# Optimization experiments

Measured on AMD Instinct MI355X. Metric: run time of the kernel, lower is better.

The kernel has to match this reference:

```python
import jax, jax.numpy as jnp
import numpy as np

N = 1_000_000          # points
C_IN = 10              # decorated point features
C_OUT = 64             # pillar feature channels
S = 30_000             # number of pillars (segments)
EPS = 1e-3             # BatchNorm1d eps


def setup_inputs() -> dict:
    key = jax.random.key(0)
    ks = jax.random.split(key, 8)
    inputs = jax.random.normal(ks[0], (N, C_IN), dtype=jnp.float32)
    # every pillar gets ~N/S points; sorted, all segments non-empty
    unq_inv = jnp.sort(jnp.arange(N, dtype=jnp.int32) % S)
    W_lin = jax.random.normal(ks[1], (C_OUT, C_IN), dtype=jnp.float32) * 0.3
    gamma = 1.0 + 0.1 * jax.random.normal(ks[2], (C_OUT,), dtype=jnp.float32)
    beta = 0.1 * jax.random.normal(ks[3], (C_OUT,), dtype=jnp.float32)
    dw1 = jax.random.normal(ks[4], (C_OUT,), dtype=jnp.float32) * 0.5      # depthwise 1x1 conv (groups=C)
    pw1 = jax.random.normal(ks[5], (C_OUT, C_OUT), dtype=jnp.float32) * 0.1  # pointwise 1x1 conv
    dw2 = jax.random.normal(ks[6], (C_OUT,), dtype=jnp.float32) * 0.5
    pw2 = jax.random.normal(ks[7], (C_OUT, C_OUT), dtype=jnp.float32) * 0.1
    return {"inputs": inputs, "unq_inv": unq_inv, "W_lin": W_lin,
            "gamma": gamma, "beta": beta, "dw1": dw1, "pw1": pw1,
            "dw2": dw2, "pw2": pw2}


def reference(inputs, unq_inv, W_lin, gamma, beta, dw1, pw1, dw2, pw2):
    # Linear (no bias) -> BN (training-mode batch stats) -> ReLU
    x = inputs @ W_lin.T                                   # [N, C]
    mu = jnp.mean(x, axis=0)
    var = jnp.mean(jnp.square(x - mu), axis=0)             # biased var, as torch BN
    x = (x - mu) * jax.lax.rsqrt(var + EPS) * gamma + beta
    x = jax.nn.relu(x)

    # MAFF attention: local branch (depthwise scale -> swish -> 1x1 conv)
    s = x * dw1                                            # groups=C 1x1 conv == per-channel scale
    xl = (s * jax.nn.sigmoid(s)) @ pw1.T                   # [N, C]
    # global branch: avg-pool over points -> depthwise scale -> relu -> 1x1 conv
    g = jnp.mean(x, axis=0)                                # [C]
    xg = pw2 @ jax.nn.relu(dw2 * g)                        # [C]
    wei = jax.nn.sigmoid(xl + xg)                          # broadcast [N,C] + [C]
    xi = x * (1.0 + wei)

    # segment reductions keyed by pillar id (scatter_max + scatter_sum)
    x_max = jax.ops.segment_max(xi, unq_inv, num_segments=S,
                                indices_are_sorted=True)
    x_sum = jax.ops.segment_sum(xi, unq_inv, num_segments=S,
                                indices_are_sorted=True)
    return x_max + x_sum                                   # [S, C]
```

## Files before the change

kernel.cpp:

```cpp
#include <hip/hip_runtime.h>
#include <math.h>

#define N_PTS   1000000
#define CI      10
#define C       64
#define NSEG    30000
#define BN_EPS  1e-3f
#define FROFF   31104

#define MSTR 7
#define GOFF 512
#define GSTR 8
#define CTRI 961

using f32x4 = __attribute__((ext_vector_type(4))) float;
using s16x8 = __attribute__((ext_vector_type(8))) short;

__device__ inline short f2bf(float x) {
    unsigned u = __float_as_uint(x);
    unsigned r = (u + 0x7fffu + ((u >> 16) & 1u)) >> 16;
    return (short)r;
}
__device__ inline unsigned pack_trunc(float lo, float hi) {
    return (__float_as_uint(hi) & 0xffff0000u) | (__float_as_uint(lo) >> 16);
}
__device__ inline float frcp(float x) { return __builtin_amdgcn_rcpf(x); }
__device__ inline void lds_fence() {
    asm volatile("s_waitcnt lgkmcnt(0)" ::: "memory");
}

struct Rows { float2 r0, r1, r2, r3; };

__global__ void __launch_bounds__(256) k_moments(const float* __restrict__ inp,
                                                 const int* __restrict__ idx,
                                                 float* __restrict__ ws,
                                                 int* __restrict__ starts) {
    const int tid = threadIdx.x;
    const int stride = gridDim.x * blockDim.x;
    float v[65];
#pragma unroll
    for (int k = 0; k < 65; ++k) v[k] = 0.f;

    int p = blockIdx.x * blockDim.x + tid;
    float2 a0, a1, a2, a3, a4;
    int ic = 0, ip = 0;
    auto ld = [&](int qq) {
        const float2* r2 = (const float2*)(inp + (size_t)qq * CI);
        a0 = r2[0]; a1 = r2[1]; a2 = r2[2]; a3 = r2[3]; a4 = r2[4];
        ic = idx[qq]; ip = (qq > 0) ? idx[qq - 1] : ic;
    };
    if (p < N_PTS) ld(p);
    while (p < N_PTS) {
        float r[CI] = {a0.x, a0.y, a1.x, a1.y, a2.x, a2.y, a3.x, a3.y, a4.x, a4.y};
        const int cc = ic, cp = ip, cq = p;
        const int pn = p + stride;
        if (pn < N_PTS) ld(pn);

#pragma unroll
        for (int i = 0; i < CI; ++i) v[i] += r[i];
        int kk = 10;
#pragma unroll
        for (int i = 0; i < CI; ++i)
#pragma unroll
            for (int j = i; j < CI; ++j) { v[kk] = fmaf(r[i], r[j], v[kk]); ++kk; }

        if (cq == 0) starts[0] = 0;
        else if (cp != cc) starts[cc] = cq;
        p = pn;
    }

#pragma unroll
    for (int k = 0; k < 65; ++k) {
#pragma unroll
        for (int off = 32; off >= 1; off >>= 1)
            v[k] += __shfl_xor(v[k], off, 64);
    }
    __shared__ float red[4 * 65];
    const int wv = tid >> 6, ln = tid & 63;
    if (ln == 0) {
#pragma unroll
        for (int k = 0; k < 65; ++k) red[wv * 65 + k] = v[k];
    }
    __syncthreads();
    if (tid < 65)
        atomicAdd(&ws[MSTR * tid],
                  red[tid] + red[65 + tid] + red[130 + tid] + red[195 + tid]);
}

#define GS_TP 500
__global__ void __launch_bounds__(256) k_gstats(const float* __restrict__ inp,
                                                const float* __restrict__ W,
                                                const float* __restrict__ gamma,
                                                const float* __restrict__ beta,
                                                const float* __restrict__ dw1,
                                                const float* __restrict__ pw1,
                                                const float* __restrict__ dw2,
                                                const float* __restrict__ pw2,
                                                float* __restrict__ ws) {
    const int tid  = threadIdx.x;
    const int wv   = tid >> 6;
    const int lane = tid & 63;
    const int m = lane & 15;
    const int q = lane >> 4;
    const float inv_n = 1.f / (float)N_PTS;

    __shared__ float tile[GS_TP * CI];
    __shared__ float wp[C * CI];
    __shared__ float bsh[C];
    __shared__ float red[4 * 64];

    {
        const float4* src = (const float4*)(inp + (size_t)blockIdx.x * GS_TP * CI);
        float4* dst = (float4*)tile;
        for (int i = tid; i < GS_TP * CI / 4; i += 256) dst[i] = src[i];
    }

    float wa[CI], b;
    {
        float w[CI];
#pragma unroll
        for (int i = 0; i < CI; ++i) w[i] = W[lane * CI + i];
        float mu = 0.f;
#pragma unroll
        for (int i = 0; i < CI; ++i) mu = fmaf(w[i], ws[MSTR * i], mu);
        mu *= inv_n;
        float ex2 = 0.f;
        int kk = 10;
#pragma unroll
        for (int i = 0; i < CI; ++i)
#pragma unroll
            for (int j = i; j < CI; ++j) {
                float mm = ws[MSTR * kk];
                float t = w[i] * w[j] * mm;
                ex2 += (i == j) ? t : 2.f * t;
                ++kk;
            }
        ex2 *= inv_n;
        float var = ex2 - mu * mu;
        float rstd = rsqrtf(var + BN_EPS);
        float a = rstd * gamma[lane];
        b = beta[lane] - mu * a;
#pragma unroll
        for (int i = 0; i < CI; ++i) wa[i] = a * w[i];
        if (wv == 0) {
            bsh[lane] = b;
#pragma unroll
            for (int i = 0; i < CI; ++i) wp[lane * CI + i] = wa[i];
        }
    }
    __syncthreads();

    float g0 = 0.f, g1 = 0.f;
    const int ps = wv * 125;
    for (int p = ps; p < ps + 124; p += 2) {
        const float* r0 = &tile[p * CI];
        const float* r1 = &tile[(p + 1) * CI];
        float acc0 = b, acc1 = b;
#pragma unroll
        for (int i2 = 0; i2 < 5; ++i2) {
            float2 u0 = *(const float2*)(r0 + 2 * i2);
            float2 u1 = *(const float2*)(r1 + 2 * i2);
            acc0 = fmaf(wa[2 * i2], u0.x, fmaf(wa[2 * i2 + 1], u0.y, acc0));
            acc1 = fmaf(wa[2 * i2], u1.x, fmaf(wa[2 * i2 + 1], u1.y, acc1));
        }
        g0 += fmaxf(acc0, 0.f);
        g1 += fmaxf(acc1, 0.f);
    }
    {
        const float* r0 = &tile[(ps + 124) * CI];
        float acc0 = b;
#pragma unroll
        for (int i2 = 0; i2 < 5; ++i2) {
            float2 u0 = *(const float2*)(r0 + 2 * i2);
            acc0 = fmaf(wa[2 * i2], u0.x, fmaf(wa[2 * i2 + 1], u0.y, acc0));
        }
        g0 += fmaxf(acc0, 0.f);
    }

    red[wv * 64 + lane] = g0 + g1;
    __syncthreads();
    if (tid < 64)
        atomicAdd(&ws[GOFF + GSTR * tid],
                  red[tid] + red[64 + tid] + red[128 + tid] + red[192 + tid]);

    __shared__ int lastf;
    __syncthreads();
    if (tid == 0) {
        __threadfence();
        int old = atomicAdd((int*)ws + CTRI, 1);
        lastf = (old == (int)gridDim.x - 1);
    }
    __syncthreads();
    if (!lastf) return;
    __threadfence();

    __shared__ float T[C], XG[C];
    if (tid < 64)
        T[tid] = fmaxf(dw2[tid] * (ws[GOFF + GSTR * tid] * inv_n), 0.f);
    __syncthreads();
    if (tid < 64) {
        float acc = 0.f;
#pragma unroll
        for (int k = 0; k < C; ++k) acc = fmaf(pw2[tid * C + k], T[k], acc);
        XG[tid] = acc;
    }
    __syncthreads();

    if (tid < 64) {
        float4* FR = (float4*)(ws + FROFF);
        union { float4 f; s16x8 v; } u;

#pragma unroll
        for (int nt = 0; nt < 4; ++nt) {
            s16x8 tt;
#pragma unroll
            for (int j = 0; j < 8; ++j) {
                int k = 8 * q + j;
                tt[j] = (k < CI) ? f2bf(wp[(nt * 16 + m) * CI + k]) : (short)0;
            }
            u.v = tt; FR[nt * 64 + lane] = u.f;
        }
#pragma unroll
        for (int nt = 0; nt < 4; ++nt)
#pragma unroll
            for (int kc = 0; kc < 2; ++kc) {
                const float* src = pw1 + (nt * 16 + m) * C + kc * 32 + q * 8;
                float4 p0 = *(const float4*)src, p1 = *(const float4*)(src + 4);
                s16x8 tt;
                tt[0] = f2bf(p0.x); tt[1] = f2bf(p0.y); tt[2] = f2bf(p0.z); tt[3] = f2bf(p0.w);
                tt[4] = f2bf(p1.x); tt[5] = f2bf(p1.y); tt[6] = f2bf(p1.z); tt[7] = f2bf(p1.w);
                u.v = tt; FR[(4 + nt * 2 + kc) * 64 + lane] = u.f;
            }
        float4 f;
        f.x = bsh[m]; f.y = bsh[16 + m]; f.z = bsh[32 + m]; f.w = bsh[48 + m];
        FR[12 * 64 + lane] = f;
        f.x = dw1[m]; f.y = dw1[16 + m]; f.z = dw1[32 + m]; f.w = dw1[48 + m];
        FR[13 * 64 + lane] = f;
        f.x = XG[m]; f.y = XG[16 + m]; f.z = XG[32 + m]; f.w = XG[48 + m];
        FR[14 * 64 + lane] = f;
    }
}

#define LD 68
#define SEGW 2
__global__ void __launch_bounds__(128) k_main(const float* __restrict__ inp,
                                              const float* __restrict__ ws,
                                              const int* __restrict__ starts,
                                              float* __restrict__ out) {
    const int tid  = threadIdx.x;
    const int wv   = tid >> 6;
    const int lane = tid & 63;
    const int m = lane & 15;
    const int q = lane >> 4;
    const f32x4 zero = {0.f, 0.f, 0.f, 0.f};

    const float4* FR = (const float4*)(ws + FROFF);
    union { float4 f; s16x8 v; } u;
    s16x8 wfr[4];
#pragma unroll
    for (int nt = 0; nt < 4; ++nt) { u.f = FR[nt * 64 + lane]; wfr[nt] = u.v; }
    s16x8 bfr[4][2];
#pragma unroll
    for (int nt = 0; nt < 4; ++nt)
#pragma unroll
        for (int kc = 0; kc < 2; ++kc) { u.f = FR[(4 + nt * 2 + kc) * 64 + lane]; bfr[nt][kc] = u.v; }
    const float4 bb4  = FR[12 * 64 + lane];
    const float4 d14  = FR[13 * 64 + lane];
    const float4 xg4  = FR[14 * 64 + lane];
    const float bb[4]  = {bb4.x, bb4.y, bb4.z, bb4.w};
    const float d1v[4] = {d14.x, d14.y, d14.z, d14.w};
    const float xgv[4] = {xg4.x, xg4.y, xg4.z, xg4.w};

    __shared__ float sb[2][16 * LD];
    float* my = sb[wv];

    const int w  = blockIdx.x * 2 + wv;
    const int s0 = w * SEGW;

    int st1 = starts[s0 + 1];
    int st2 = (s0 + 2 < NSEG) ? starts[s0 + 2] : N_PTS;
    const int start   = starts[s0];
    const int end_all = st2;

    int cur = s0;
    int end_cur = st1;

    float sm[4]  = {0.f, 0.f, 0.f, 0.f};
    float mxv[4] = {-INFINITY, -INFINITY, -INFINITY, -INFINITY};

    auto flushseg = [&](int s) {
#pragma unroll
        for (int nt = 0; nt < 4; ++nt) {
            sm[nt] += __shfl_xor(sm[nt], 16, 64);
            sm[nt] += __shfl_xor(sm[nt], 32, 64);
            mxv[nt] = fmaxf(mxv[nt], __shfl_xor(mxv[nt], 16, 64));
            mxv[nt] = fmaxf(mxv[nt], __shfl_xor(mxv[nt], 32, 64));
        }
        float S = sm[0], M = mxv[0];
        if (q == 1) { S = sm[1]; M = mxv[1]; }
        if (q == 2) { S = sm[2]; M = mxv[2]; }
        if (q == 3) { S = sm[3]; M = mxv[3]; }
        out[(size_t)s * C + lane] = S + M;
#pragma unroll
        for (int nt = 0; nt < 4; ++nt) { sm[nt] = 0.f; mxv[nt] = -INFINITY; }
    };

    auto loadrows = [&](int pb) -> Rows {
        Rows R;
        R.r0 = R.r1 = R.r2 = R.r3 = make_float2(0.f, 0.f);
        const float* row = inp + (size_t)min(pb + m, N_PTS - 1) * CI;
        if (q == 0) {
            R.r0 = *(const float2*)(row);     R.r1 = *(const float2*)(row + 2);
            R.r2 = *(const float2*)(row + 4); R.r3 = *(const float2*)(row + 6);
        } else if (q == 1) {
            R.r0 = *(const float2*)(row + 8);
        }
        return R;
    };

    Rows A = loadrows(start);
    Rows B = (start + 16 < end_all) ? loadrows(start + 16) : A;

    for (int base = start; base < end_all; base += 16) {
        Rows L = A;
        A = B;
        if (base + 32 < end_all) B = loadrows(base + 32);

        const int nb = min(16, end_all - base);

        union { s16x8 v; unsigned uu[4]; } t;
        t.v = s16x8{0, 0, 0, 0, 0, 0, 0, 0};
        if (q < 2) t.uu[0] = pack_trunc(L.r0.x, L.r0.y);
        if (q == 0) {
            t.uu[1] = pack_trunc(L.r1.x, L.r1.y);
            t.uu[2] = pack_trunc(L.r2.x, L.r2.y);
            t.uu[3] = pack_trunc(L.r3.x, L.r3.y);
        }

        f32x4 xt[4];
#pragma unroll
        for (int nt = 0; nt < 4; ++nt)
            xt[nt] = __builtin_amdgcn_mfma_f32_16x16x32_bf16(t.v, wfr[nt], zero, 0, 0, 0);

        float xn[4][4];
#pragma unroll
        for (int nt = 0; nt < 4; ++nt)
#pragma unroll
            for (int r = 0; r < 4; ++r) {
                float x = fmaxf(xt[nt][r] + bb[nt], 0.f);
                xn[nt][r] = x;
                float sg = x * d1v[nt];
                float sw = sg * frcp(1.f + __expf(-sg));
                my[(4 * q + r) * LD + nt * 16 + m] = sw;
            }
        lds_fence();

        s16x8 av[2];
#pragma unroll
        for (int kc = 0; kc < 2; ++kc) {
            const float* src = &my[m * LD + kc * 32 + q * 8];
            float4 p0 = *(const float4*)src;
            float4 p1 = *(const float4*)(src + 4);
            union { s16x8 v; unsigned uu[4]; } tt;
            tt.uu[0] = pack_trunc(p0.x, p0.y);
            tt.uu[1] = pack_trunc(p0.z, p0.w);
            tt.uu[2] = pack_trunc(p1.x, p1.y);
            tt.uu[3] = pack_trunc(p1.z, p1.w);
            av[kc] = tt.v;
        }

        f32x4 xi[4];
#pragma unroll
        for (int nt = 0; nt < 4; ++nt) {
            xi[nt] = __builtin_amdgcn_mfma_f32_16x16x32_bf16(av[0], bfr[nt][0], zero, 0, 0, 0);
            xi[nt] = __builtin_amdgcn_mfma_f32_16x16x32_bf16(av[1], bfr[nt][1], xi[nt], 0, 0, 0);
        }
        lds_fence();

#pragma unroll
        for (int nt = 0; nt < 4; ++nt)
#pragma unroll
            for (int r = 0; r < 4; ++r) {
                float v   = xi[nt][r] + xgv[nt];
                float wei = frcp(1.f + __expf(-v));
                float x   = xn[nt][r];
                xi[nt][r] = fmaf(x, wei, x);
            }

        const int fin = base + nb;
        if (fin <= end_cur) {
            if (nb == 16) {
#pragma unroll
                for (int nt = 0; nt < 4; ++nt)
#pragma unroll
                    for (int r = 0; r < 4; ++r) {
                        sm[nt] += xi[nt][r];
                        mxv[nt] = fmaxf(mxv[nt], xi[nt][r]);
                    }
            } else {
#pragma unroll
                for (int nt = 0; nt < 4; ++nt)
#pragma unroll
                    for (int r = 0; r < 4; ++r) {
                        bool act = (4 * q + r) < nb;
                        sm[nt] += act ? xi[nt][r] : 0.f;
                        mxv[nt] = fmaxf(mxv[nt], act ? xi[nt][r] : -INFINITY);
                    }
            }
            if (fin == end_cur) { flushseg(cur); ++cur; end_cur = st2; }
        } else {
            const int B = end_cur - base;
#pragma unroll
            for (int nt = 0; nt < 4; ++nt)
#pragma unroll
                for (int r = 0; r < 4; ++r) {
                    bool act = (4 * q + r) < B;
                    sm[nt] += act ? xi[nt][r] : 0.f;
                    mxv[nt] = fmaxf(mxv[nt], act ? xi[nt][r] : -INFINITY);
                }
            flushseg(cur); ++cur;
#pragma unroll
            for (int nt = 0; nt < 4; ++nt)
#pragma unroll
                for (int r = 0; r < 4; ++r) {
                    int pt = 4 * q + r;
                    bool act = (pt >= B) && (pt < nb);
                    sm[nt] += act ? xi[nt][r] : 0.f;
                    mxv[nt] = fmaxf(mxv[nt], act ? xi[nt][r] : -INFINITY);
                }
            end_cur = st2;
        }
    }
}

extern "C" void kernel_launch(void* const* d_in, const int* in_sizes, int n_in,
                              void* d_out, int out_size, void* d_ws, size_t ws_size,
                              hipStream_t stream) {
    const float* inp   = (const float*)d_in[0];
    const int*   unq   = (const int*)d_in[1];
    const float* W     = (const float*)d_in[2];
    const float* gamma = (const float*)d_in[3];
    const float* beta  = (const float*)d_in[4];
    const float* dw1   = (const float*)d_in[5];
    const float* pw1   = (const float*)d_in[6];
    const float* dw2   = (const float*)d_in[7];
    const float* pw2   = (const float*)d_in[8];
    float* out = (float*)d_out;
    float* ws  = (float*)d_ws;
    int* starts = (int*)ws + 1024;

    hipMemsetAsync(ws, 0, 1024 * sizeof(float), stream);

    k_moments <<<1024, 256, 0, stream>>>(inp, unq, ws, starts);
    k_gstats  <<<2000, 256, 0, stream>>>(inp, W, gamma, beta, dw1, pw1, dw2, pw2, ws);
    k_main    <<<7500, 128, 0, stream>>>(inp, ws, starts, out);
}
```

Measured before the change: 298.2 us.

## Stream gstats input through registers with readlane broadcast instead of LDS tile

The global-mean pass no longer stages a 500-point tile in shared memory. Each wave now loads 64 input rows into registers, one row per lane, and walks a grid-stride loop over batches with a one-batch register prefetch. It broadcasts each point's features with readlane to compute the per-channel ReLU sums. This removes the LDS copy and the block barrier and overlaps the global loads with compute. In exchange it issues many scalar readlane operations per point, and with the grid cut to 1024 blocks some waves get one more batch than others.

```diff
diff --git a/kernel.cpp b/kernel.cpp
--- a/kernel.cpp
+++ b/kernel.cpp
@@ -27,6 +27,9 @@
 __device__ inline float frcp(float x) { return __builtin_amdgcn_rcpf(x); }
 __device__ inline void lds_fence() {
     asm volatile("s_waitcnt lgkmcnt(0)" ::: "memory");
+}
+__device__ inline float bcastlane(float x, int l) {
+    return __int_as_float(__builtin_amdgcn_readlane(__float_as_int(x), l));
 }
 
 struct Rows { float2 r0, r1, r2, r3; };
@@ -87,7 +90,6 @@
                   red[tid] + red[65 + tid] + red[130 + tid] + red[195 + tid]);
 }
 
-#define GS_TP 500
 __global__ void __launch_bounds__(256) k_gstats(const float* __restrict__ inp,
                                                 const float* __restrict__ W,
                                                 const float* __restrict__ gamma,
@@ -104,16 +106,9 @@
     const int q = lane >> 4;
     const float inv_n = 1.f / (float)N_PTS;
 
-    __shared__ float tile[GS_TP * CI];
     __shared__ float wp[C * CI];
     __shared__ float bsh[C];
     __shared__ float red[4 * 64];
-
-    {
-        const float4* src = (const float4*)(inp + (size_t)blockIdx.x * GS_TP * CI);
-        float4* dst = (float4*)tile;
-        for (int i = tid; i < GS_TP * CI / 4; i += 256) dst[i] = src[i];
-    }
 
     float wa[CI], b;
     {
@@ -148,33 +143,37 @@
             for (int i = 0; i < CI; ++i) wp[lane * CI + i] = wa[i];
         }
     }
-    __syncthreads();
+
+    const int wid = blockIdx.x * 4 + wv;
+    const int nw  = gridDim.x * 4;
+    const int NBATCH = N_PTS / 64;
+
+    float r0[CI], r1[CI];
+    auto ldrow = [&](float* r, int bt) {
+        const float2* s = (const float2*)(inp + ((size_t)bt * 64 + lane) * CI);
+        float2 x0 = s[0], x1 = s[1], x2 = s[2], x3 = s[3], x4 = s[4];
+        r[0] = x0.x; r[1] = x0.y; r[2] = x1.x; r[3] = x1.y; r[4] = x2.x;
+        r[5] = x2.y; r[6] = x3.x; r[7] = x3.y; r[8] = x4.x; r[9] = x4.y;
+    };
 
     float g0 = 0.f, g1 = 0.f;
-    const int ps = wv * 125;
-    for (int p = ps; p < ps + 124; p += 2) {
-        const float* r0 = &tile[p * CI];
-        const float* r1 = &tile[(p + 1) * CI];
-        float acc0 = b, acc1 = b;
-#pragma unroll
-        for (int i2 = 0; i2 < 5; ++i2) {
-            float2 u0 = *(const float2*)(r0 + 2 * i2);
-            float2 u1 = *(const float2*)(r1 + 2 * i2);
-            acc0 = fmaf(wa[2 * i2], u0.x, fmaf(wa[2 * i2 + 1], u0.y, acc0));
-            acc1 = fmaf(wa[2 * i2], u1.x, fmaf(wa[2 * i2 + 1], u1.y, acc1));
-        }
-        g0 += fmaxf(acc0, 0.f);
-        g1 += fmaxf(acc1, 0.f);
-    }
-    {
-        const float* r0 = &tile[(ps + 124) * CI];
-        float acc0 = b;
-#pragma unroll
-        for (int i2 = 0; i2 < 5; ++i2) {
-            float2 u0 = *(const float2*)(r0 + 2 * i2);
-            acc0 = fmaf(wa[2 * i2], u0.x, fmaf(wa[2 * i2 + 1], u0.y, acc0));
-        }
-        g0 += fmaxf(acc0, 0.f);
+    if (wid < NBATCH) ldrow(r0, wid);
+    for (int bt = wid; bt < NBATCH; bt += nw) {
+        if (bt + nw < NBATCH) ldrow(r1, bt + nw);
+
+#pragma unroll 4
+        for (int p = 0; p < 64; p += 2) {
+            float acc0 = b, acc1 = b;
+#pragma unroll
+            for (int i = 0; i < CI; ++i) {
+                acc0 = fmaf(wa[i], bcastlane(r0[i], p), acc0);
+                acc1 = fmaf(wa[i], bcastlane(r0[i], p + 1), acc1);
+            }
+            g0 += fmaxf(acc0, 0.f);
+            g1 += fmaxf(acc1, 0.f);
+        }
+#pragma unroll
+        for (int i = 0; i < CI; ++i) r0[i] = r1[i];
     }
 
     red[wv * 64 + lane] = g0 + g1;
@@ -452,6 +451,6 @@
     hipMemsetAsync(ws, 0, 1024 * sizeof(float), stream);
 
     k_moments <<<1024, 256, 0, stream>>>(inp, unq, ws, starts);
-    k_gstats  <<<2000, 256, 0, stream>>>(inp, W, gamma, beta, dw1, pw1, dw2, pw2, ws);
+    k_gstats  <<<1024, 256, 0, stream>>>(inp, W, gamma, beta, dw1, pw1, dw2, pw2, ws);
     k_main    <<<7500, 128, 0, stream>>>(inp, ws, starts, out);
 }
```

Result: faster. 283.2 us (-5.0%).
